# Performance work log

Measured on AMD Instinct MI355X. Metric: run time of the kernel, lower is better.

Reference implementation:

```python
import jax, jax.numpy as jnp
import numpy as np

N_NODES = 50000
N_EDGES = 800000
IN_CH = 64
HID = 128
OUT_CH = 1
NUM_LAYERS = 3
NUM_TIMESTEPS = 3
EDGE_DIM = 25
NUM_GRAPHS = 1024
NEG = 0.01  # leaky_relu negative slope (torch default & GATConv arg)


def leaky(v):
    return jnp.where(v >= 0, v, NEG * v)


def seg_softmax(a, idx, n):
    # PyG softmax: exp(a - max_per_segment) / (sum_per_segment + 1e-16)
    m = jax.ops.segment_max(a, idx, num_segments=n)
    m = jnp.where(jnp.isfinite(m), m, 0.0)  # guard empty segments
    e = jnp.exp(a - m[idx])
    s = jax.ops.segment_sum(e, idx, num_segments=n)
    return e / (s[idx] + 1e-16)


def gru(inp, h, Wih, Whh, bih, bhh):
    gi = inp @ Wih.T + bih
    gh = h @ Whh.T + bhh
    ir, iz, inn = jnp.split(gi, 3, axis=-1)
    hr, hz, hn = jnp.split(gh, 3, axis=-1)
    r = jax.nn.sigmoid(ir + hr)
    z = jax.nn.sigmoid(iz + hz)
    n = jnp.tanh(inn + r * hn)
    return (1.0 - z) * n + z * h


def setup_inputs() -> dict:
    key = jax.random.key(0)
    ks = iter(jax.random.split(key, 40))

    def nrm(shape, s=0.05):
        return jax.random.normal(next(ks), shape, dtype=jnp.float32) * s

    L = NUM_LAYERS - 1
    H3 = 3 * HID
    inp = dict(
        x=jax.random.normal(next(ks), (N_NODES, IN_CH), dtype=jnp.float32),
        edge_index=jax.random.randint(next(ks), (2, N_EDGES), 0, N_NODES),
        batch=jnp.sort(jax.random.randint(next(ks), (N_NODES,), 0, NUM_GRAPHS)),
        W1=nrm((HID, IN_CH)), b1=jnp.zeros((HID,), jnp.float32),
        Wg1=nrm((HID, HID + EDGE_DIM)), att_l=nrm((HID,)), att_r=nrm((HID,)),
        Wg2=nrm((HID, HID)), bg=jnp.zeros((HID,), jnp.float32),
        Wih0=nrm((H3, HID)), Whh0=nrm((H3, HID)),
        bih0=jnp.zeros((H3,), jnp.float32), bhh0=jnp.zeros((H3,), jnp.float32),
        Wa=nrm((L, HID, HID)), att_src_a=nrm((L, HID)), att_dst_a=nrm((L, HID)),
        ba=jnp.zeros((L, HID), jnp.float32),
        Wih_a=nrm((L, H3, HID)), Whh_a=nrm((L, H3, HID)),
        bih_a=jnp.zeros((L, H3), jnp.float32), bhh_a=jnp.zeros((L, H3), jnp.float32),
        Wm=nrm((HID, HID)), att_src_m=nrm((HID,)), att_dst_m=nrm((HID,)),
        bm=jnp.zeros((HID,), jnp.float32),
        Wih_m=nrm((H3, HID)), Whh_m=nrm((H3, HID)),
        bih_m=jnp.zeros((H3,), jnp.float32), bhh_m=jnp.zeros((H3,), jnp.float32),
        W2=nrm((OUT_CH, HID)), b2=jnp.zeros((OUT_CH,), jnp.float32),
    )
    return inp


def reference(x, edge_index, batch, W1, b1, Wg1, att_l, att_r, Wg2, bg,
              Wih0, Whh0, bih0, bhh0, Wa, att_src_a, att_dst_a, ba,
              Wih_a, Whh_a, bih_a, bhh_a, Wm, att_src_m, att_dst_m, bm,
              Wih_m, Whh_m, bih_m, bhh_m, W2, b2):
    N = x.shape[0]
    E = edge_index.shape[1]
    src, dst = edge_index[0], edge_index[1]  # j -> i, aggregate at i=dst
    edge_attr = jnp.ones((E, EDGE_DIM), dtype=x.dtype)  # built inside original forward

    x = leaky(x @ W1.T + b1)

    # GATEConv: edge-feature-aware attention, sum aggregation
    xe = leaky(jnp.concatenate([x[src], edge_attr], axis=-1) @ Wg1.T)  # [E, H]
    a = seg_softmax(leaky(xe @ att_l + (x @ att_r)[dst]), dst, N)
    msg = (x[src] @ Wg2.T) * a[:, None]
    h = jax.nn.elu(jax.ops.segment_sum(msg, dst, num_segments=N) + bg)
    x = jax.nn.relu(gru(h, x, Wih0, Whh0, bih0, bhh0))

    # (num_layers - 1) GATConv + GRU atom updates
    for l in range(NUM_LAYERS - 1):
        xt = x @ Wa[l].T
        a = seg_softmax(leaky((xt @ att_src_a[l])[src] + (xt @ att_dst_a[l])[dst]), dst, N)
        h = jax.nn.elu(jax.ops.segment_sum(xt[src] * a[:, None], dst, num_segments=N) + ba[l])
        x = jax.nn.relu(gru(h, x, Wih_a[l], Whh_a[l], bih_a[l], bhh_a[l]))

    # attentive readout: bipartite GATConv node->molecule over num_timesteps
    out = jax.nn.relu(jax.ops.segment_sum(x, batch, num_segments=NUM_GRAPHS))
    xt = x @ Wm.T                 # shared lin for src (fixed across timesteps)
    a_src = xt @ att_src_m        # [N]
    for _ in range(NUM_TIMESTEPS):
        ot = out @ Wm.T           # shared lin for dst
        a = seg_softmax(leaky(a_src + (ot @ att_dst_m)[batch]), batch, NUM_GRAPHS)
        h = jax.nn.elu(jax.ops.segment_sum(xt * a[:, None], batch, num_segments=NUM_GRAPHS) + bm)
        out = jax.nn.relu(gru(h, out, Wih_m, Whh_m, bih_m, bhh_m))

    return out @ W2.T + b2
```

## Files before the change

kernel.cpp:

```cpp
#include <hip/hip_runtime.h>
#include <math.h>

#define NN 50000
#define NE 800000
#define NG 1024
#define HID 128

typedef __attribute__((ext_vector_type(8))) short short8;
typedef __attribute__((ext_vector_type(4))) unsigned short ushort4v;
typedef __attribute__((ext_vector_type(4))) float f32x4;

__device__ __forceinline__ float leakyf(float v){ return v >= 0.f ? v : 0.01f*v; }
__device__ __forceinline__ float frcp(float x){ return __builtin_amdgcn_rcpf(x); }
__device__ __forceinline__ float fsigm(float v){ return frcp(1.f + __expf(-v)); }
__device__ __forceinline__ float ftanh(float v){ return 1.f - 2.f*frcp(1.f + __expf(2.f*v)); }
__device__ __forceinline__ float eluf(float v){ return v > 0.f ? v : __expf(v) - 1.f; }
__device__ __forceinline__ unsigned short bf16rne(float f){
  union { float f; unsigned u; } v; v.f = f;
  return (unsigned short)((v.u + 0x7FFFu + ((v.u >> 16) & 1u)) >> 16);
}
__device__ __forceinline__ float bf2f(unsigned short h){
  union { unsigned u; float f; } v; v.u = ((unsigned)h) << 16; return v.f;
}
__device__ __forceinline__ short8 cvt8(const float* a){
  short8 r;
#pragma unroll
  for (int j=0;j<8;j++) r[j] = (short)bf16rne(a[j]);
  return r;
}

__global__ __launch_bounds__(256)
void pack_all(const float* W1, const float* Wg1, const float* Wg2, const float* Wa,
              const float* Wm, const float* Wih0, const float* Whh0,
              const float* Wih_a, const float* Whh_a, const float* Wih_m,
              const float* Whh_m, unsigned short* __restrict__ dst)
{
  int m = (int)blockIdx.y;
  int t = (int)blockIdx.x*4 + ((int)threadIdx.x>>6);
  int l = (int)threadIdx.x & 63;
  const float* src; int stride=128, M=128, K=128; size_t doff;
  switch(m){
    case 0:  src=W1;    stride=64;  K=64;  doff=0;      break;
    case 1:  src=Wg1;   stride=153;        doff=8192;   break;
    case 2:  src=Wg2;                      doff=24576;  break;
    case 3:  src=Wa;                       doff=40960;  break;
    case 4:  src=Wa+16384;                 doff=57344;  break;
    case 5:  src=Wm;                       doff=73728;  break;
    case 6:  src=Wih0;  M=384;             doff=90112;  break;
    case 7:  src=Whh0;  M=384;             doff=139264; break;
    case 8:  src=Wih_a; M=384;             doff=188416; break;
    case 9:  src=Whh_a; M=384;             doff=237568; break;
    case 10: src=Wih_a+49152; M=384;       doff=286720; break;
    case 11: src=Whh_a+49152; M=384;       doff=335872; break;
    case 12: src=Wih_m; M=384;             doff=385024; break;
    default: src=Whh_m; M=384;             doff=434176; break;
  }
  int tk = K/32;
  if (t >= (M/16)*tk) return;
  int ct = t / tk, kc = t % tk;
  int row = ct*16 + (l&15);
  int col = kc*32 + ((l>>4)<<3);
  unsigned short o[8];
#pragma unroll
  for (int j=0;j<8;j++) o[j] = bf16rne(src[(size_t)row*stride + col + j]);
  ushort4v* d = (ushort4v*)(dst + doff + (((size_t)t*64 + l)<<3));
  ushort4v d0; d0.x=o[0]; d0.y=o[1]; d0.z=o[2]; d0.w=o[3];
  ushort4v d1; d1.x=o[4]; d1.y=o[5]; d1.z=o[6]; d1.w=o[7];
  d[0]=d0; d[1]=d1;
}

__global__ __launch_bounds__(256)
void gemm_f32(const float* __restrict__ A, const unsigned short* __restrict__ Wp,
              const float* __restrict__ bias, float* __restrict__ Cf,
              unsigned short* __restrict__ Cb, int rows, int act)
{
  constexpr int K = 64, KC = 2;
  const int tid=(int)threadIdx.x, w=tid>>6, l=tid&63;
  const int fr=l&15, fq=l>>4;
  const int rt=w>>1, ch=w&1;
  const int bn = (int)blockIdx.x*32;
  const int ar = bn + rt*16 + fr;
  f32x4 acc[4];
#pragma unroll
  for (int j=0;j<4;j++) acc[j] = (f32x4){0.f,0.f,0.f,0.f};
#pragma unroll
  for (int kc=0;kc<KC;kc++){
    float a8[8];
    if (ar < rows){
      *(float4*)&a8[0] = *(const float4*)(A + (size_t)ar*K + kc*32 + fq*8);
      *(float4*)&a8[4] = *(const float4*)(A + (size_t)ar*K + kc*32 + fq*8 + 4);
    } else {
#pragma unroll
      for (int j=0;j<8;j++) a8[j]=0.f;
    }
    short8 fa = cvt8(a8);
#pragma unroll
    for (int j=0;j<4;j++){
      const short8 bfr = *(const short8*)(Wp + ((((size_t)(ch*4+j)*KC + kc)*64 + l)<<3));
      acc[j] = __builtin_amdgcn_mfma_f32_16x16x32_bf16(fa, bfr, acc[j], 0, 0, 0);
    }
  }
#pragma unroll
  for (int j=0;j<4;j++){
    int c = ch*64 + j*16 + fr;
    float bv = bias ? bias[c] : 0.f;
#pragma unroll
    for (int r4=0;r4<4;r4++){
      float o = acc[j][r4] + bv;
      if (act) o = leakyf(o);
      int r = bn + rt*16 + fq*4 + r4;
      if (r < rows){
        Cf[(size_t)r*HID + c] = o;
        Cb[(size_t)r*HID + c] = bf16rne(o);
      }
    }
  }
}

__global__ __launch_bounds__(256)
void gemm_b16(const unsigned short* __restrict__ Ab, const unsigned short* __restrict__ Wp,
              const float* __restrict__ bias, unsigned short* __restrict__ Cb,
              const float* __restrict__ v1, const float* __restrict__ v2,
              float* __restrict__ s1, float* __restrict__ s2, int rows, int act)
{
  __shared__ float sd1[2][32];
  __shared__ float sd2[2][32];
  constexpr int KC = 4;
  const int tid=(int)threadIdx.x, w=tid>>6, l=tid&63;
  const int fr=l&15, fq=l>>4;
  const int rt=w>>1, ch=w&1;
  const int bn = (int)blockIdx.x*32;
  const int ar = bn + rt*16 + fr;
  f32x4 acc[4];
#pragma unroll
  for (int j=0;j<4;j++) acc[j] = (f32x4){0.f,0.f,0.f,0.f};
#pragma unroll
  for (int kc=0;kc<KC;kc++){
    short8 fa;
    if (ar < rows) fa = *(const short8*)(Ab + (size_t)ar*HID + kc*32 + fq*8);
    else { short8 z = {0,0,0,0,0,0,0,0}; fa = z; }
#pragma unroll
    for (int j=0;j<4;j++){
      const short8 bfr = *(const short8*)(Wp + ((((size_t)(ch*4+j)*KC + kc)*64 + l)<<3));
      acc[j] = __builtin_amdgcn_mfma_f32_16x16x32_bf16(fa, bfr, acc[j], 0, 0, 0);
    }
  }
  float dp1[4]={0.f,0.f,0.f,0.f}, dp2[4]={0.f,0.f,0.f,0.f};
#pragma unroll
  for (int j=0;j<4;j++){
    int c = ch*64 + j*16 + fr;
    float bv = bias ? bias[c] : 0.f;
    float w1 = v1 ? v1[c] : 0.f;
    float w2 = v2 ? v2[c] : 0.f;
#pragma unroll
    for (int r4=0;r4<4;r4++){
      float o = acc[j][r4] + bv;
      if (act) o = leakyf(o);
      dp1[r4] += o*w1; dp2[r4] += o*w2;
      int r = bn + rt*16 + fq*4 + r4;
      if (r < rows && Cb) Cb[(size_t)r*HID + c] = bf16rne(o);
    }
  }
  if (v1){
#pragma unroll
    for (int r4=0;r4<4;r4++){
#pragma unroll
      for (int m=1;m<16;m<<=1){ dp1[r4] += __shfl_xor(dp1[r4], m); dp2[r4] += __shfl_xor(dp2[r4], m); }
    }
    if (fr==0){
#pragma unroll
      for (int r4=0;r4<4;r4++){
        sd1[ch][rt*16 + fq*4 + r4] = dp1[r4];
        sd2[ch][rt*16 + fq*4 + r4] = dp2[r4];
      }
    }
    __syncthreads();
    if (tid < 32){
      int r = bn + tid;
      if (r < rows) s1[r] = sd1[0][tid] + sd1[1][tid];
    } else if (v2 && tid < 64){
      int r = bn + tid - 32;
      if (r < rows) s2[r] = sd2[0][tid-32] + sd2[1][tid-32];
    }
  }
}

__global__ __launch_bounds__(256)
void gemm_gate(const unsigned short* __restrict__ Ab,
               const unsigned short* __restrict__ W1p, const unsigned short* __restrict__ W2p,
               const float* __restrict__ cg, const float* __restrict__ attl,
               const float* __restrict__ attr,
               unsigned short* __restrict__ Cb,
               float* __restrict__ s1, float* __restrict__ s2, int rows)
{
  __shared__ float sd1[2][32];
  constexpr int KC = 4;
  const int tid=(int)threadIdx.x, w=tid>>6, l=tid&63;
  const int fr=l&15, fq=l>>4;
  const int rt=w>>1, ch=w&1;
  const int bn = (int)blockIdx.x*32;
  const int ar = bn + rt*16 + fr;
  f32x4 acc1[4], acc2[4];
#pragma unroll
  for (int j=0;j<4;j++){ acc1[j]=(f32x4){0,0,0,0}; acc2[j]=(f32x4){0,0,0,0}; }
  float pa = 0.f;
#pragma unroll
  for (int kc=0;kc<KC;kc++){
    short8 fa;
    if (ar < rows) fa = *(const short8*)(Ab + (size_t)ar*HID + kc*32 + fq*8);
    else { short8 z = {0,0,0,0,0,0,0,0}; fa = z; }
    if (ch==0){
      float4 t0 = *(const float4*)(attr + kc*32 + fq*8);
      float4 t1 = *(const float4*)(attr + kc*32 + fq*8 + 4);
      pa += bf2f((unsigned short)fa[0])*t0.x + bf2f((unsigned short)fa[1])*t0.y
          + bf2f((unsigned short)fa[2])*t0.z + bf2f((unsigned short)fa[3])*t0.w
          + bf2f((unsigned short)fa[4])*t1.x + bf2f((unsigned short)fa[5])*t1.y
          + bf2f((unsigned short)fa[6])*t1.z + bf2f((unsigned short)fa[7])*t1.w;
    }
#pragma unroll
    for (int j=0;j<4;j++){
      size_t wo = ((((size_t)(ch*4+j)*KC + kc)*64 + l)<<3);
      acc1[j] = __builtin_amdgcn_mfma_f32_16x16x32_bf16(fa, *(const short8*)(W1p + wo), acc1[j], 0, 0, 0);
      acc2[j] = __builtin_amdgcn_mfma_f32_16x16x32_bf16(fa, *(const short8*)(W2p + wo), acc2[j], 0, 0, 0);
    }
  }
  float dp1[4]={0.f,0.f,0.f,0.f};
#pragma unroll
  for (int j=0;j<4;j++){
    int c = ch*64 + j*16 + fr;
    float bv = cg[c];
    float w1 = attl[c];
#pragma unroll
    for (int r4=0;r4<4;r4++){
      float o1 = leakyf(acc1[j][r4] + bv);
      dp1[r4] += o1*w1;
      int r = bn + rt*16 + fq*4 + r4;
      if (r < rows) Cb[(size_t)r*HID + c] = bf16rne(acc2[j][r4]);
    }
  }
#pragma unroll
  for (int r4=0;r4<4;r4++){
#pragma unroll
    for (int m=1;m<16;m<<=1) dp1[r4] += __shfl_xor(dp1[r4], m);
  }
  if (fr==0){
#pragma unroll
    for (int r4=0;r4<4;r4++) sd1[ch][rt*16 + fq*4 + r4] = dp1[r4];
  }
  __syncthreads();
  if (tid < 32){
    int r = bn + tid;
    if (r < rows) s1[r] = sd1[0][tid] + sd1[1][tid];
  }
  if (ch==0){
    pa += __shfl_xor(pa, 16); pa += __shfl_xor(pa, 32);
    if (fq==0){
      int r = bn + rt*16 + fr;
      if (r < rows) s2[r] = pa;
    }
  }
}

#define GRU_TPB 4
__global__ __launch_bounds__(512, 2)
void fused_gru(const unsigned short* __restrict__ Ahb, const unsigned short* __restrict__ Axb,
               const float* __restrict__ Axf,
               const unsigned short* __restrict__ Wi, const unsigned short* __restrict__ Wh,
               const float* __restrict__ bih, const float* __restrict__ bhh,
               float* __restrict__ outf, unsigned short* __restrict__ outb, int tiles)
{
  const int tid=(int)threadIdx.x, w=tid>>6, l=tid&63;
  const int fr=l&15, fq=l>>4;
  short8 wi_r[3][4], wh_r[3][4];
#pragma unroll
  for (int g=0;g<3;g++)
#pragma unroll
    for (int kc=0;kc<4;kc++){
      size_t o = ((((size_t)(g*8 + w)*4 + kc)*64 + l)<<3);
      wi_r[g][kc] = *(const short8*)(Wi + o);
      wh_r[g][kc] = *(const short8*)(Wh + o);
    }
  const int c0 = w*16 + fr;
  float bi0=bih[c0], bi1=bih[c0+128], bi2=bih[c0+256];
  float bh0=bhh[c0], bh1=bhh[c0+128], bh2=bhh[c0+256];

  int rt = (int)blockIdx.x*GRU_TPB;
  int rt_end = min(rt + GRU_TPB, tiles);
  if (rt >= tiles) return;
  short8 fa[4], fx[4];
  {
    const int arow = rt*16 + fr;
#pragma unroll
    for (int kc=0;kc<4;kc++){
      fa[kc] = *(const short8*)(Ahb + (size_t)arow*HID + kc*32 + fq*8);
      fx[kc] = *(const short8*)(Axb + (size_t)arow*HID + kc*32 + fq*8);
    }
  }
  for (; rt < rt_end; rt++){
    short8 nfa[4], nfx[4];
    if (rt+1 < rt_end){
      const int arow = (rt+1)*16 + fr;
#pragma unroll
      for (int kc=0;kc<4;kc++){
        nfa[kc] = *(const short8*)(Ahb + (size_t)arow*HID + kc*32 + fq*8);
        nfx[kc] = *(const short8*)(Axb + (size_t)arow*HID + kc*32 + fq*8);
      }
    }
    float hv[4];
#pragma unroll
    for (int r4=0;r4<4;r4++) hv[r4] = Axf[(size_t)(rt*16 + fq*4 + r4)*HID + c0];

    f32x4 ai0={0,0,0,0}, ai1={0,0,0,0}, ai2={0,0,0,0};
    f32x4 ah0={0,0,0,0}, ah1={0,0,0,0}, ah2={0,0,0,0};
#pragma unroll
    for (int kc=0;kc<4;kc++){
      ai0 = __builtin_amdgcn_mfma_f32_16x16x32_bf16(fa[kc], wi_r[0][kc], ai0, 0, 0, 0);
      ai1 = __builtin_amdgcn_mfma_f32_16x16x32_bf16(fa[kc], wi_r[1][kc], ai1, 0, 0, 0);
      ai2 = __builtin_amdgcn_mfma_f32_16x16x32_bf16(fa[kc], wi_r[2][kc], ai2, 0, 0, 0);
      ah0 = __builtin_amdgcn_mfma_f32_16x16x32_bf16(fx[kc], wh_r[0][kc], ah0, 0, 0, 0);
      ah1 = __builtin_amdgcn_mfma_f32_16x16x32_bf16(fx[kc], wh_r[1][kc], ah1, 0, 0, 0);
      ah2 = __builtin_amdgcn_mfma_f32_16x16x32_bf16(fx[kc], wh_r[2][kc], ah2, 0, 0, 0);
    }
#pragma unroll
    for (int r4=0;r4<4;r4++){
      int row = rt*16 + fq*4 + r4;
      float rr = fsigm(ai0[r4] + bi0 + ah0[r4] + bh0);
      float zz = fsigm(ai1[r4] + bi1 + ah1[r4] + bh1);
      float nn = ftanh(ai2[r4] + bi2 + rr*(ah2[r4] + bh2));
      float o = fmaxf((1.f - zz)*nn + zz*hv[r4], 0.f);
      outf[(size_t)row*HID + c0] = o;
      outb[(size_t)row*HID + c0] = bf16rne(o);
    }
#pragma unroll
    for (int kc=0;kc<4;kc++){ fa[kc]=nfa[kc]; fx[kc]=nfx[kc]; }
  }
}

__global__ __launch_bounds__(256)
void rowdot(const float* __restrict__ A, const float* __restrict__ v,
            const float* __restrict__ bias, float* __restrict__ out, int rows)
{
  int wave = (int)((blockIdx.x * blockDim.x + threadIdx.x) >> 6);
  int lane = (int)(threadIdx.x & 63);
  if (wave >= rows) return;
  float2 a  = ((const float2*)(A + (size_t)wave*HID))[lane];
  float2 vv = ((const float2*)v)[lane];
  float s = a.x*vv.x + a.y*vv.y;
  for (int off=32; off; off>>=1) s += __shfl_down(s, off);
  if (lane==0) out[wave] = s + (bias ? bias[0] : 0.f);
}

__global__ void colvec(const float* __restrict__ W, const float* __restrict__ v,
                       float* __restrict__ out)
{
  int k = (int)threadIdx.x;
  float s = 0.f;
  for (int j=0;j<HID;j++) s += W[j*HID+k]*v[j];
  out[k] = s;
}

__global__ void prep_cg(const float* __restrict__ Wg1, float* __restrict__ cg){
  int j = (int)threadIdx.x;
  float s = 0.f;
  for (int k=128;k<153;k++) s += Wg1[j*153+k];
  cg[j] = s;
}

__global__ void count_kernel(const int* __restrict__ idx, int* __restrict__ cnt, int n){
  int i = (int)(blockIdx.x*blockDim.x + threadIdx.x);
  if (i < n) atomicAdd(&cnt[idx[i]], 1);
}

__global__ __launch_bounds__(1024)
void scan_blocks(const int* __restrict__ cnt, int* __restrict__ off,
                 int* __restrict__ tot, int n)
{
  __shared__ int buf[1024];
  int i = (int)(blockIdx.x*1024 + threadIdx.x);
  int v = (i<n)? cnt[i] : 0;
  buf[threadIdx.x] = v;
  __syncthreads();
  for (int s=1;s<1024;s<<=1){
    int t = ((int)threadIdx.x >= s) ? buf[threadIdx.x - s] : 0;
    __syncthreads();
    buf[threadIdx.x] += t;
    __syncthreads();
  }
  if (i<n) off[i] = buf[threadIdx.x] - v;
  if (threadIdx.x==1023) tot[blockIdx.x] = buf[1023];
}

__global__ void scan_tot(int* __restrict__ tot, int* __restrict__ off_end, int nb){
  int lane = (int)threadIdx.x;
  int orig = (lane<nb)? tot[lane] : 0;
  int v = orig;
  for (int s=1;s<64;s<<=1){ int t = __shfl_up(v, s); if (lane>=s) v += t; }
  int total = __shfl(v, 63);
  if (lane<nb) tot[lane] = v - orig;
  if (lane==0) *off_end = total;
}

__global__ void scan_add(int* __restrict__ off, const int* __restrict__ tot, int n){
  int i = (int)(blockIdx.x*blockDim.x + threadIdx.x);
  if (i<n) off[i] += tot[i>>10];
}

__global__ void fill_kernel(const int* __restrict__ src, const int* __restrict__ dst,
                            const int* __restrict__ off, int* __restrict__ fill,
                            int* __restrict__ ssrc, int n){
  int e = (int)(blockIdx.x*blockDim.x + threadIdx.x);
  if (e < n){
    int d = dst[e];
    int p = off[d] + atomicAdd(&fill[d], 1);
    __builtin_nontemporal_store(src[e], &ssrc[p]);
  }
}

__global__ void graph_bounds(const int* __restrict__ batch, int* __restrict__ goff){
  int g = (int)(blockIdx.x*blockDim.x + threadIdx.x);
  if (g > NG) return;
  int lo=0, hi=NN;
  while (lo<hi){ int mid=(lo+hi)>>1; if (batch[mid] < g) lo=mid+1; else hi=mid; }
  goff[g] = lo;
}

__global__ __launch_bounds__(256)
void agg_edges(const int* __restrict__ off, const int* __restrict__ ssrc,
               const float* __restrict__ ls, const float* __restrict__ ld,
               const unsigned short* __restrict__ Mrows, const float* __restrict__ bias,
               unsigned short* __restrict__ outb, int n)
{
  __shared__ float wbuf[4][64];
  __shared__ int   sbuf[4][64];
  const int ws = (int)(threadIdx.x >> 6);
  int node = (int)((blockIdx.x * blockDim.x + threadIdx.x) >> 6);
  int lane = (int)(threadIdx.x & 63);
  if (node >= n) return;
  int e0 = off[node], e1 = off[node+1];
  float ldv = ld[node];
  const int g4 = lane >> 4, cl = lane & 15;
  float denom = 0.f;
  float acc[8] = {0.f,0.f,0.f,0.f,0.f,0.f,0.f,0.f};
  for (int j0=e0; j0<e1; j0+=64){
    int cnt = min(64, e1-j0);
    float wv = 0.f; int sc = 0;
    if (lane < cnt){
      sc = ssrc[j0+lane];
      wv = __expf(leakyf(ls[sc]+ldv));
    }
    denom += wv;
    wbuf[ws][lane] = wv;
    sbuf[ws][lane] = sc;
#pragma unroll 2
    for (int k4=0;k4<cnt;k4+=4){
      float wk = wbuf[ws][k4+g4];
      int  sck = sbuf[ws][k4+g4];
      uint4 mm = *(const uint4*)(Mrows + (size_t)sck*HID + cl*8);
      acc[0] += wk*bf2f((unsigned short)(mm.x&0xffff));
      acc[1] += wk*bf2f((unsigned short)(mm.x>>16));
      acc[2] += wk*bf2f((unsigned short)(mm.y&0xffff));
      acc[3] += wk*bf2f((unsigned short)(mm.y>>16));
      acc[4] += wk*bf2f((unsigned short)(mm.z&0xffff));
      acc[5] += wk*bf2f((unsigned short)(mm.z>>16));
      acc[6] += wk*bf2f((unsigned short)(mm.w&0xffff));
      acc[7] += wk*bf2f((unsigned short)(mm.w>>16));
    }
  }
#pragma unroll
  for (int j=0;j<8;j++){ acc[j] += __shfl_xor(acc[j], 16); acc[j] += __shfl_xor(acc[j], 32); }
  for (int o=32;o;o>>=1) denom += __shfl_xor(denom, o);
  if (g4==0){
    float inv = frcp(denom + 1e-16f);
    float4 b0 = *(const float4*)(bias + cl*8);
    float4 b1 = *(const float4*)(bias + cl*8 + 4);
    float o0=eluf(acc[0]*inv+b0.x), o1=eluf(acc[1]*inv+b0.y);
    float o2=eluf(acc[2]*inv+b0.z), o3=eluf(acc[3]*inv+b0.w);
    float o4=eluf(acc[4]*inv+b1.x), o5=eluf(acc[5]*inv+b1.y);
    float o6=eluf(acc[6]*inv+b1.z), o7=eluf(acc[7]*inv+b1.w);
    uint4 u;
    u.x = (unsigned)bf16rne(o0) | ((unsigned)bf16rne(o1)<<16);
    u.y = (unsigned)bf16rne(o2) | ((unsigned)bf16rne(o3)<<16);
    u.z = (unsigned)bf16rne(o4) | ((unsigned)bf16rne(o5)<<16);
    u.w = (unsigned)bf16rne(o6) | ((unsigned)bf16rne(o7)<<16);
    *(uint4*)(outb + (size_t)node*HID + cl*8) = u;
  }
}

__global__ __launch_bounds__(128)
void graph_sum(const int* __restrict__ goff, const float* __restrict__ X,
               float* __restrict__ outf, unsigned short* __restrict__ outb)
{
  int g = (int)blockIdx.x;
  int c = (int)threadIdx.x;
  int n0 = goff[g], n1 = goff[g+1];
  float a0=0.f, a1=0.f, a2=0.f, a3=0.f;
  int n = n0;
  for (; n+4 <= n1; n += 4){
    a0 += X[(size_t)(n+0)*HID + c];
    a1 += X[(size_t)(n+1)*HID + c];
    a2 += X[(size_t)(n+2)*HID + c];
    a3 += X[(size_t)(n+3)*HID + c];
  }
  for (; n < n1; ++n) a0 += X[(size_t)n*HID + c];
  float o = fmaxf((a0+a1)+(a2+a3), 0.f);
  outf[(size_t)g*HID + c] = o;
  outb[(size_t)g*HID + c] = bf16rne(o);
}

__global__ __launch_bounds__(256)
void graph_soft2(const int* __restrict__ goff, const float* __restrict__ asrc,
                 const float* __restrict__ gout, const float* __restrict__ vmd,
                 const unsigned short* __restrict__ Xt, const float* __restrict__ bias,
                 unsigned short* __restrict__ outb)
{
  __shared__ float wbuf[4][64];
  const int ws = (int)(threadIdx.x >> 6);
  int g = (int)((blockIdx.x*blockDim.x + threadIdx.x) >> 6);
  int lane = (int)(threadIdx.x & 63);
  if (g >= NG) return;
  float2 ov = ((const float2*)(gout + (size_t)g*HID))[lane];
  float2 vv = ((const float2*)vmd)[lane];
  float ad = ov.x*vv.x + ov.y*vv.y;
  for (int o=32;o;o>>=1) ad += __shfl_xor(ad, o);
  int n0 = goff[g], n1 = goff[g+1];
  const int g4 = lane >> 4, cl = lane & 15;
  float denom = 0.f;
  float acc[8] = {0.f,0.f,0.f,0.f,0.f,0.f,0.f,0.f};
  for (int j0=n0; j0<n1; j0+=64){
    int cnt = min(64, n1-j0);
    float wv = 0.f;
    if (lane < cnt) wv = __expf(leakyf(asrc[j0+lane]+ad));
    denom += wv;
    wbuf[ws][lane] = wv;
#pragma unroll 2
    for (int k4=0;k4<cnt;k4+=4){
      float wk = wbuf[ws][k4+g4];
      int rowi = min(j0 + k4 + g4, n1 - 1);
      uint4 mm = *(const uint4*)(Xt + (size_t)rowi*HID + cl*8);
      acc[0] += wk*bf2f((unsigned short)(mm.x&0xffff));
      acc[1] += wk*bf2f((unsigned short)(mm.x>>16));
      acc[2] += wk*bf2f((unsigned short)(mm.y&0xffff));
      acc[3] += wk*bf2f((unsigned short)(mm.y>>16));
      acc[4] += wk*bf2f((unsigned short)(mm.z&0xffff));
      acc[5] += wk*bf2f((unsigned short)(mm.z>>16));
      acc[6] += wk*bf2f((unsigned short)(mm.w&0xffff));
      acc[7] += wk*bf2f((unsigned short)(mm.w>>16));
    }
  }
#pragma unroll
  for (int j=0;j<8;j++){ acc[j] += __shfl_xor(acc[j], 16); acc[j] += __shfl_xor(acc[j], 32); }
  for (int o=32;o;o>>=1) denom += __shfl_xor(denom, o);
  if (g4==0){
    float inv = frcp(denom + 1e-16f);
    float4 b0 = *(const float4*)(bias + cl*8);
    float4 b1 = *(const float4*)(bias + cl*8 + 4);
    float o0=eluf(acc[0]*inv+b0.x), o1=eluf(acc[1]*inv+b0.y);
    float o2=eluf(acc[2]*inv+b0.z), o3=eluf(acc[3]*inv+b0.w);
    float o4=eluf(acc[4]*inv+b1.x), o5=eluf(acc[5]*inv+b1.y);
    float o6=eluf(acc[6]*inv+b1.z), o7=eluf(acc[7]*inv+b1.w);
    uint4 u;
    u.x = (unsigned)bf16rne(o0) | ((unsigned)bf16rne(o1)<<16);
    u.y = (unsigned)bf16rne(o2) | ((unsigned)bf16rne(o3)<<16);
    u.z = (unsigned)bf16rne(o4) | ((unsigned)bf16rne(o5)<<16);
    u.w = (unsigned)bf16rne(o6) | ((unsigned)bf16rne(o7)<<16);
    *(uint4*)(outb + (size_t)g*HID + cl*8) = u;
  }
}

extern "C" void kernel_launch(void* const* d_in, const int* in_sizes, int n_in,
                              void* d_out, int out_size, void* d_ws, size_t ws_size,
                              hipStream_t stream)
{
  const float* x_in  = (const float*)d_in[0];
  const int*   ei    = (const int*)d_in[1];
  const int*   batch = (const int*)d_in[2];
  const float* W1    = (const float*)d_in[3];
  const float* b1    = (const float*)d_in[4];
  const float* Wg1   = (const float*)d_in[5];
  const float* att_l = (const float*)d_in[6];
  const float* att_r = (const float*)d_in[7];
  const float* Wg2   = (const float*)d_in[8];
  const float* bg    = (const float*)d_in[9];
  const float* Wih0  = (const float*)d_in[10];
  const float* Whh0  = (const float*)d_in[11];
  const float* bih0  = (const float*)d_in[12];
  const float* bhh0  = (const float*)d_in[13];
  const float* Wa    = (const float*)d_in[14];
  const float* att_src_a = (const float*)d_in[15];
  const float* att_dst_a = (const float*)d_in[16];
  const float* ba    = (const float*)d_in[17];
  const float* Wih_a = (const float*)d_in[18];
  const float* Whh_a = (const float*)d_in[19];
  const float* bih_a = (const float*)d_in[20];
  const float* bhh_a = (const float*)d_in[21];
  const float* Wm    = (const float*)d_in[22];
  const float* att_src_m = (const float*)d_in[23];
  const float* att_dst_m = (const float*)d_in[24];
  const float* bm    = (const float*)d_in[25];
  const float* Wih_m = (const float*)d_in[26];
  const float* Whh_m = (const float*)d_in[27];
  const float* bih_m = (const float*)d_in[28];
  const float* bhh_m = (const float*)d_in[29];
  const float* W2    = (const float*)d_in[30];
  const float* b2    = (const float*)d_in[31];
  (void)in_sizes; (void)n_in; (void)out_size; (void)ws_size;

  char* wsb = (char*)d_ws;
  size_t off = 0;
  auto alloc = [&](size_t bytes)->void* {
    void* p = wsb + off;
    off += (bytes + 255) & ~(size_t)255;
    return p;
  };
  float* f_x   = (float*)alloc((size_t)NN*HID*4);
  float* f_y   = (float*)alloc((size_t)NN*HID*4);
  unsigned short* f_xb = (unsigned short*)alloc((size_t)NN*HID*2);
  unsigned short* f_yb = (unsigned short*)alloc((size_t)NN*HID*2);
  unsigned short* f_h  = (unsigned short*)alloc((size_t)NN*HID*2);
  unsigned short* f_t  = (unsigned short*)alloc((size_t)NN*HID*2);
  float* f_s1  = (float*)alloc((size_t)NN*4);
  float* f_s2  = (float*)alloc((size_t)NN*4);
  float* g_of0 = (float*)alloc((size_t)NG*HID*4);
  float* g_of1 = (float*)alloc((size_t)NG*HID*4);
  unsigned short* g_ob0 = (unsigned short*)alloc((size_t)NG*HID*2);
  unsigned short* g_ob1 = (unsigned short*)alloc((size_t)NG*HID*2);
  unsigned short* g_hb  = (unsigned short*)alloc((size_t)NG*HID*2);
  float* w_cg  = (float*)alloc((size_t)HID*4);
  float* w_vmd = (float*)alloc((size_t)HID*4);
  unsigned short* w_pack = (unsigned short*)alloc((size_t)483328*2);
  int* i_cnt   = (int*)alloc((size_t)NN*4);
  int* i_off   = (int*)alloc((size_t)(NN+1)*4);
  int* i_fill  = (int*)alloc((size_t)NN*4);
  int* i_src   = (int*)alloc((size_t)NE*4);
  int* i_tot   = (int*)alloc((size_t)64*4);
  int* i_goff  = (int*)alloc((size_t)(NG+1)*4);

  const unsigned short* pk_W1   = w_pack + 0;
  const unsigned short* pk_g1   = w_pack + 8192;
  const unsigned short* pk_g2   = w_pack + 24576;
  const unsigned short* pk_wa0  = w_pack + 40960;
  const unsigned short* pk_wa1  = w_pack + 57344;
  const unsigned short* pk_wm   = w_pack + 73728;
  const unsigned short* pk_wih0 = w_pack + 90112;
  const unsigned short* pk_whh0 = w_pack + 139264;
  const unsigned short* pk_wiha0= w_pack + 188416;
  const unsigned short* pk_whha0= w_pack + 237568;
  const unsigned short* pk_wiha1= w_pack + 286720;
  const unsigned short* pk_whha1= w_pack + 335872;
  const unsigned short* pk_wihm = w_pack + 385024;
  const unsigned short* pk_whhm = w_pack + 434176;

  const int* e_src = ei;
  const int* e_dst = ei + NE;

  hipMemsetAsync(i_cnt, 0, (size_t)NN*4, stream);
  hipMemsetAsync(i_fill, 0, (size_t)NN*4, stream);

  const int NB = (NN + 1023)/1024;
  count_kernel<<<(NE+255)/256,256,0,stream>>>(e_dst, i_cnt, NE);
  scan_blocks<<<NB,1024,0,stream>>>(i_cnt, i_off, i_tot, NN);
  scan_tot<<<1,64,0,stream>>>(i_tot, i_off+NN, NB);
  scan_add<<<(NN+255)/256,256,0,stream>>>(i_off, i_tot, NN);
  fill_kernel<<<(NE+255)/256,256,0,stream>>>(e_src, e_dst, i_off, i_fill, i_src, NE);
  graph_bounds<<<(NG+1+255)/256,256,0,stream>>>(batch, i_goff);
  prep_cg<<<1,128,0,stream>>>(Wg1, w_cg);
  colvec<<<1,128,0,stream>>>(Wm, att_dst_m, w_vmd);
  pack_all<<<dim3(24,14),256,0,stream>>>(W1, Wg1, Wg2, Wa, Wm, Wih0, Whh0,
                                         Wih_a, Whh_a, Wih_m, Whh_m, w_pack);

  const int GB = (NN+31)/32;
  const int NT = NN/16;
  const int FB = (NT+GRU_TPB-1)/GRU_TPB;
  const int GT = NG/16;
  const int wavegrid_g = (NG*64)/256;

  gemm_f32<<<GB,256,0,stream>>>(x_in, pk_W1, b1, f_x, f_xb, NN, 1);

  float* curf = f_x;  unsigned short* curb = f_xb;
  float* nxtf = f_y;  unsigned short* nxtb = f_yb;

  gemm_gate<<<GB,256,0,stream>>>(curb, pk_g1, pk_g2, w_cg, att_l, att_r,
                                 f_t, f_s1, f_s2, NN);
  agg_edges<<<(NN+3)/4,256,0,stream>>>(i_off, i_src, f_s1, f_s2, f_t, bg, f_h, NN);
  fused_gru<<<FB,512,0,stream>>>(f_h, curb, curf, pk_wih0, pk_whh0, bih0, bhh0,
                                 nxtf, nxtb, NT);
  { float* t=curf; curf=nxtf; nxtf=t; unsigned short* tb=curb; curb=nxtb; nxtb=tb; }

  for (int l=0;l<2;l++){
    gemm_b16<<<GB,256,0,stream>>>(curb, l ? pk_wa1 : pk_wa0, nullptr, f_t,
                                  att_src_a + l*HID, att_dst_a + l*HID,
                                  f_s1, f_s2, NN, 0);
    agg_edges<<<(NN+3)/4,256,0,stream>>>(i_off, i_src, f_s1, f_s2, f_t, ba + l*HID, f_h, NN);
    fused_gru<<<FB,512,0,stream>>>(f_h, curb, curf,
                                   l ? pk_wiha1 : pk_wiha0, l ? pk_whha1 : pk_whha0,
                                   bih_a + l*384, bhh_a + l*384, nxtf, nxtb, NT);
    { float* t=curf; curf=nxtf; nxtf=t; unsigned short* tb=curb; curb=nxtb; nxtb=tb; }
  }

  graph_sum<<<NG,128,0,stream>>>(i_goff, curf, g_of0, g_ob0);
  gemm_b16<<<GB,256,0,stream>>>(curb, pk_wm, nullptr, f_t,
                                att_src_m, nullptr, f_s1, nullptr, NN, 0);
  float* gcf = g_of0; unsigned short* gcb = g_ob0;
  float* gnf = g_of1; unsigned short* gnb = g_ob1;
  for (int t=0;t<3;t++){
    graph_soft2<<<wavegrid_g,256,0,stream>>>(i_goff, f_s1, gcf, w_vmd, f_t, bm, g_hb);
    fused_gru<<<(GT+GRU_TPB-1)/GRU_TPB,512,0,stream>>>(g_hb, gcb, gcf, pk_wihm, pk_whhm,
                                                       bih_m, bhh_m, gnf, gnb, GT);
    { float* tf=gcf; gcf=gnf; gnf=tf; unsigned short* tb=gcb; gcb=gnb; gnb=tb; }
  }

  rowdot<<<wavegrid_g,256,0,stream>>>(gcf, W2, b2, (float*)d_out, NG);
}
```

Measured before the change: 620.4 us.

## Fuse attentive readout timesteps, GRU and output into one per-graph kernel

After: 618.6 us. No clear change (-0.3%).

```diff
diff --git a/kernel.cpp b/kernel.cpp
--- a/kernel.cpp
+++ b/kernel.cpp
@@ -32,8 +32,8 @@
 __global__ __launch_bounds__(256)
 void pack_all(const float* W1, const float* Wg1, const float* Wg2, const float* Wa,
               const float* Wm, const float* Wih0, const float* Whh0,
-              const float* Wih_a, const float* Whh_a, const float* Wih_m,
-              const float* Whh_m, unsigned short* __restrict__ dst)
+              const float* Wih_a, const float* Whh_a,
+              unsigned short* __restrict__ dst)
 {
   int m = (int)blockIdx.y;
   int t = (int)blockIdx.x*4 + ((int)threadIdx.x>>6);
@@ -51,9 +51,7 @@
     case 8:  src=Wih_a; M=384;             doff=188416; break;
     case 9:  src=Whh_a; M=384;             doff=237568; break;
     case 10: src=Wih_a+49152; M=384;       doff=286720; break;
-    case 11: src=Whh_a+49152; M=384;       doff=335872; break;
-    case 12: src=Wih_m; M=384;             doff=385024; break;
-    default: src=Whh_m; M=384;             doff=434176; break;
+    default: src=Whh_a+49152; M=384;       doff=335872; break;
   }
   int tk = K/32;
   if (t >= (M/16)*tk) return;
@@ -67,6 +65,15 @@
   ushort4v d0; d0.x=o[0]; d0.y=o[1]; d0.z=o[2]; d0.w=o[3];
   ushort4v d1; d1.x=o[4]; d1.y=o[5]; d1.z=o[6]; d1.w=o[7];
   d[0]=d0; d[1]=d1;
+}
+
+__global__ void pack_t(const float* __restrict__ Wi, const float* __restrict__ Wh,
+                       unsigned short* __restrict__ Wit, unsigned short* __restrict__ Wht)
+{
+  int k = (int)blockIdx.x;
+  int cg = (int)threadIdx.x + (int)blockIdx.y*128;
+  Wit[(size_t)k*384 + cg] = bf16rne(Wi[(size_t)cg*128 + k]);
+  Wht[(size_t)k*384 + cg] = bf16rne(Wh[(size_t)cg*128 + k]);
 }
 
 __global__ __launch_bounds__(256)
@@ -336,20 +343,6 @@
   }
 }
 
-__global__ __launch_bounds__(256)
-void rowdot(const float* __restrict__ A, const float* __restrict__ v,
-            const float* __restrict__ bias, float* __restrict__ out, int rows)
-{
-  int wave = (int)((blockIdx.x * blockDim.x + threadIdx.x) >> 6);
-  int lane = (int)(threadIdx.x & 63);
-  if (wave >= rows) return;
-  float2 a  = ((const float2*)(A + (size_t)wave*HID))[lane];
-  float2 vv = ((const float2*)v)[lane];
-  float s = a.x*vv.x + a.y*vv.y;
-  for (int off=32; off; off>>=1) s += __shfl_down(s, off);
-  if (lane==0) out[wave] = s + (bias ? bias[0] : 0.f);
-}
-
 __global__ void colvec(const float* __restrict__ W, const float* __restrict__ v,
                        float* __restrict__ out)
 {
@@ -400,19 +393,22 @@
   if (lane==0) *off_end = total;
 }
 
-__global__ void scan_add(int* __restrict__ off, const int* __restrict__ tot, int n){
+__global__ void scan_add(int* __restrict__ off, int* __restrict__ off_mut,
+                         const int* __restrict__ tot, int n){
   int i = (int)(blockIdx.x*blockDim.x + threadIdx.x);
-  if (i<n) off[i] += tot[i>>10];
+  if (i<n){
+    int v = off[i] + tot[i>>10];
+    off[i] = v;
+    off_mut[i] = v;
+  }
 }
 
 __global__ void fill_kernel(const int* __restrict__ src, const int* __restrict__ dst,
-                            const int* __restrict__ off, int* __restrict__ fill,
-                            int* __restrict__ ssrc, int n){
+                            int* __restrict__ off_mut, int* __restrict__ ssrc, int n){
   int e = (int)(blockIdx.x*blockDim.x + threadIdx.x);
   if (e < n){
-    int d = dst[e];
-    int p = off[d] + atomicAdd(&fill[d], 1);
-    __builtin_nontemporal_store(src[e], &ssrc[p]);
+    int p = atomicAdd(&off_mut[dst[e]], 1);
+    ssrc[p] = src[e];
   }
 }
 
@@ -487,84 +483,65 @@
 }
 
 __global__ __launch_bounds__(128)
-void graph_sum(const int* __restrict__ goff, const float* __restrict__ X,
-               float* __restrict__ outf, unsigned short* __restrict__ outb)
-{
-  int g = (int)blockIdx.x;
-  int c = (int)threadIdx.x;
-  int n0 = goff[g], n1 = goff[g+1];
-  float a0=0.f, a1=0.f, a2=0.f, a3=0.f;
+void readout_all(const int* __restrict__ goff, const float* __restrict__ X,
+                 const float* __restrict__ asrc, const unsigned short* __restrict__ Xt,
+                 const float* __restrict__ vmd, const float* __restrict__ bm_,
+                 const unsigned short* __restrict__ Wit, const unsigned short* __restrict__ Wht,
+                 const float* __restrict__ bih, const float* __restrict__ bhh,
+                 const float* __restrict__ W2, const float* __restrict__ b2,
+                 float* __restrict__ dout)
+{
+  __shared__ float sh_h[128];
+  __shared__ float sh_o[128];
+  __shared__ float sred[2];
+  const int g = (int)blockIdx.x, c = (int)threadIdx.x;
+  const int n0 = goff[g], n1 = goff[g+1];
+  float a0=0.f,a1=0.f,a2=0.f,a3=0.f;
   int n = n0;
-  for (; n+4 <= n1; n += 4){
-    a0 += X[(size_t)(n+0)*HID + c];
-    a1 += X[(size_t)(n+1)*HID + c];
-    a2 += X[(size_t)(n+2)*HID + c];
-    a3 += X[(size_t)(n+3)*HID + c];
-  }
-  for (; n < n1; ++n) a0 += X[(size_t)n*HID + c];
-  float o = fmaxf((a0+a1)+(a2+a3), 0.f);
-  outf[(size_t)g*HID + c] = o;
-  outb[(size_t)g*HID + c] = bf16rne(o);
-}
-
-__global__ __launch_bounds__(256)
-void graph_soft2(const int* __restrict__ goff, const float* __restrict__ asrc,
-                 const float* __restrict__ gout, const float* __restrict__ vmd,
-                 const unsigned short* __restrict__ Xt, const float* __restrict__ bias,
-                 unsigned short* __restrict__ outb)
-{
-  __shared__ float wbuf[4][64];
-  const int ws = (int)(threadIdx.x >> 6);
-  int g = (int)((blockIdx.x*blockDim.x + threadIdx.x) >> 6);
-  int lane = (int)(threadIdx.x & 63);
-  if (g >= NG) return;
-  float2 ov = ((const float2*)(gout + (size_t)g*HID))[lane];
-  float2 vv = ((const float2*)vmd)[lane];
-  float ad = ov.x*vv.x + ov.y*vv.y;
-  for (int o=32;o;o>>=1) ad += __shfl_xor(ad, o);
-  int n0 = goff[g], n1 = goff[g+1];
-  const int g4 = lane >> 4, cl = lane & 15;
-  float denom = 0.f;
-  float acc[8] = {0.f,0.f,0.f,0.f,0.f,0.f,0.f,0.f};
-  for (int j0=n0; j0<n1; j0+=64){
-    int cnt = min(64, n1-j0);
-    float wv = 0.f;
-    if (lane < cnt) wv = __expf(leakyf(asrc[j0+lane]+ad));
-    denom += wv;
-    wbuf[ws][lane] = wv;
-#pragma unroll 2
-    for (int k4=0;k4<cnt;k4+=4){
-      float wk = wbuf[ws][k4+g4];
-      int rowi = min(j0 + k4 + g4, n1 - 1);
-      uint4 mm = *(const uint4*)(Xt + (size_t)rowi*HID + cl*8);
-      acc[0] += wk*bf2f((unsigned short)(mm.x&0xffff));
-      acc[1] += wk*bf2f((unsigned short)(mm.x>>16));
-      acc[2] += wk*bf2f((unsigned short)(mm.y&0xffff));
-      acc[3] += wk*bf2f((unsigned short)(mm.y>>16));
-      acc[4] += wk*bf2f((unsigned short)(mm.z&0xffff));
-      acc[5] += wk*bf2f((unsigned short)(mm.z>>16));
-      acc[6] += wk*bf2f((unsigned short)(mm.w&0xffff));
-      acc[7] += wk*bf2f((unsigned short)(mm.w>>16));
-    }
-  }
-#pragma unroll
-  for (int j=0;j<8;j++){ acc[j] += __shfl_xor(acc[j], 16); acc[j] += __shfl_xor(acc[j], 32); }
-  for (int o=32;o;o>>=1) denom += __shfl_xor(denom, o);
-  if (g4==0){
-    float inv = frcp(denom + 1e-16f);
-    float4 b0 = *(const float4*)(bias + cl*8);
-    float4 b1 = *(const float4*)(bias + cl*8 + 4);
-    float o0=eluf(acc[0]*inv+b0.x), o1=eluf(acc[1]*inv+b0.y);
-    float o2=eluf(acc[2]*inv+b0.z), o3=eluf(acc[3]*inv+b0.w);
-    float o4=eluf(acc[4]*inv+b1.x), o5=eluf(acc[5]*inv+b1.y);
-    float o6=eluf(acc[6]*inv+b1.z), o7=eluf(acc[7]*inv+b1.w);
-    uint4 u;
-    u.x = (unsigned)bf16rne(o0) | ((unsigned)bf16rne(o1)<<16);
-    u.y = (unsigned)bf16rne(o2) | ((unsigned)bf16rne(o3)<<16);
-    u.z = (unsigned)bf16rne(o4) | ((unsigned)bf16rne(o5)<<16);
-    u.w = (unsigned)bf16rne(o6) | ((unsigned)bf16rne(o7)<<16);
-    *(uint4*)(outb + (size_t)g*HID + cl*8) = u;
-  }
+  for (; n+4<=n1; n+=4){
+    a0 += X[(size_t)(n+0)*HID+c]; a1 += X[(size_t)(n+1)*HID+c];
+    a2 += X[(size_t)(n+2)*HID+c]; a3 += X[(size_t)(n+3)*HID+c];
+  }
+  for (; n<n1; ++n) a0 += X[(size_t)n*HID+c];
+  float ov = fmaxf((a0+a1)+(a2+a3), 0.f);
+  const float bi0=bih[c], bi1=bih[c+128], bi2=bih[c+256];
+  const float bh0=bhh[c], bh1=bhh[c+128], bh2=bhh[c+256];
+  const float vm = vmd[c], bmc = bm_[c];
+  for (int t=0;t<3;t++){
+    float p = ov*vm;
+    for (int o=32;o;o>>=1) p += __shfl_down(p, o);
+    if ((c&63)==0) sred[c>>6] = p;
+    __syncthreads();
+    float ad = sred[0] + sred[1];
+    float denom = 0.f, acc = 0.f;
+    for (int nn=n0; nn<n1; ++nn){
+      float wv = __expf(leakyf(asrc[nn] + ad));
+      denom += wv;
+      acc += wv * bf2f(Xt[(size_t)nn*HID + c]);
+    }
+    float h = eluf(acc*frcp(denom + 1e-16f) + bmc);
+    __syncthreads();
+    sh_h[c] = h; sh_o[c] = ov;
+    __syncthreads();
+    float gi0=0.f,gi1=0.f,gi2=0.f,gh0=0.f,gh1=0.f,gh2=0.f;
+    for (int k=0;k<128;k++){
+      float hk = sh_h[k], ok = sh_o[k];
+      const unsigned short* wi = Wit + (size_t)k*384;
+      const unsigned short* wh = Wht + (size_t)k*384;
+      gi0 += bf2f(wi[c])*hk;  gi1 += bf2f(wi[c+128])*hk;  gi2 += bf2f(wi[c+256])*hk;
+      gh0 += bf2f(wh[c])*ok;  gh1 += bf2f(wh[c+128])*ok;  gh2 += bf2f(wh[c+256])*ok;
+    }
+    float rr = fsigm(gi0+bi0+gh0+bh0);
+    float zz = fsigm(gi1+bi1+gh1+bh1);
+    float nv = ftanh(gi2+bi2 + rr*(gh2+bh2));
+    ov = fmaxf((1.f-zz)*nv + zz*ov, 0.f);
+  }
+  float p = ov*W2[c];
+  for (int o=32;o;o>>=1) p += __shfl_down(p, o);
+  __syncthreads();
+  if ((c&63)==0) sred[c>>6] = p;
+  __syncthreads();
+  if (c==0) dout[g] = sred[0] + sred[1] + b2[0];
 }
 
 extern "C" void kernel_launch(void* const* d_in, const int* in_sizes, int n_in,
@@ -620,17 +597,14 @@
   unsigned short* f_t  = (unsigned short*)alloc((size_t)NN*HID*2);
   float* f_s1  = (float*)alloc((size_t)NN*4);
   float* f_s2  = (float*)alloc((size_t)NN*4);
-  float* g_of0 = (float*)alloc((size_t)NG*HID*4);
-  float* g_of1 = (float*)alloc((size_t)NG*HID*4);
-  unsigned short* g_ob0 = (unsigned short*)alloc((size_t)NG*HID*2);
-  unsigned short* g_ob1 = (unsigned short*)alloc((size_t)NG*HID*2);
-  unsigned short* g_hb  = (unsigned short*)alloc((size_t)NG*HID*2);
   float* w_cg  = (float*)alloc((size_t)HID*4);
   float* w_vmd = (float*)alloc((size_t)HID*4);
-  unsigned short* w_pack = (unsigned short*)alloc((size_t)483328*2);
+  unsigned short* w_pack = (unsigned short*)alloc((size_t)385024*2);
+  unsigned short* w_wit  = (unsigned short*)alloc((size_t)49152*2);
+  unsigned short* w_wht  = (unsigned short*)alloc((size_t)49152*2);
   int* i_cnt   = (int*)alloc((size_t)NN*4);
   int* i_off   = (int*)alloc((size_t)(NN+1)*4);
-  int* i_fill  = (int*)alloc((size_t)NN*4);
+  int* i_offm  = (int*)alloc((size_t)NN*4);
   int* i_src   = (int*)alloc((size_t)NE*4);
   int* i_tot   = (int*)alloc((size_t)64*4);
   int* i_goff  = (int*)alloc((size_t)(NG+1)*4);
@@ -647,32 +621,28 @@
   const unsigned short* pk_whha0= w_pack + 237568;
   const unsigned short* pk_wiha1= w_pack + 286720;
   const unsigned short* pk_whha1= w_pack + 335872;
-  const unsigned short* pk_wihm = w_pack + 385024;
-  const unsigned short* pk_whhm = w_pack + 434176;
 
   const int* e_src = ei;
   const int* e_dst = ei + NE;
 
   hipMemsetAsync(i_cnt, 0, (size_t)NN*4, stream);
-  hipMemsetAsync(i_fill, 0, (size_t)NN*4, stream);
 
   const int NB = (NN + 1023)/1024;
   count_kernel<<<(NE+255)/256,256,0,stream>>>(e_dst, i_cnt, NE);
   scan_blocks<<<NB,1024,0,stream>>>(i_cnt, i_off, i_tot, NN);
   scan_tot<<<1,64,0,stream>>>(i_tot, i_off+NN, NB);
-  scan_add<<<(NN+255)/256,256,0,stream>>>(i_off, i_tot, NN);
-  fill_kernel<<<(NE+255)/256,256,0,stream>>>(e_src, e_dst, i_off, i_fill, i_src, NE);
+  scan_add<<<(NN+255)/256,256,0,stream>>>(i_off, i_offm, i_tot, NN);
+  fill_kernel<<<(NE+255)/256,256,0,stream>>>(e_src, e_dst, i_offm, i_src, NE);
   graph_bounds<<<(NG+1+255)/256,256,0,stream>>>(batch, i_goff);
   prep_cg<<<1,128,0,stream>>>(Wg1, w_cg);
   colvec<<<1,128,0,stream>>>(Wm, att_dst_m, w_vmd);
-  pack_all<<<dim3(24,14),256,0,stream>>>(W1, Wg1, Wg2, Wa, Wm, Wih0, Whh0,
-                                         Wih_a, Whh_a, Wih_m, Whh_m, w_pack);
+  pack_all<<<dim3(24,12),256,0,stream>>>(W1, Wg1, Wg2, Wa, Wm, Wih0, Whh0,
+                                         Wih_a, Whh_a, w_pack);
+  pack_t<<<dim3(128,3),128,0,stream>>>(Wih_m, Whh_m, w_wit, w_wht);
 
   const int GB = (NN+31)/32;
   const int NT = NN/16;
   const int FB = (NT+GRU_TPB-1)/GRU_TPB;
-  const int GT = NG/16;
-  const int wavegrid_g = (NG*64)/256;
 
   gemm_f32<<<GB,256,0,stream>>>(x_in, pk_W1, b1, f_x, f_xb, NN, 1);
 
@@ -697,17 +667,9 @@
     { float* t=curf; curf=nxtf; nxtf=t; unsigned short* tb=curb; curb=nxtb; nxtb=tb; }
   }
 
-  graph_sum<<<NG,128,0,stream>>>(i_goff, curf, g_of0, g_ob0);
   gemm_b16<<<GB,256,0,stream>>>(curb, pk_wm, nullptr, f_t,
                                 att_src_m, nullptr, f_s1, nullptr, NN, 0);
-  float* gcf = g_of0; unsigned short* gcb = g_ob0;
-  float* gnf = g_of1; unsigned short* gnb = g_ob1;
-  for (int t=0;t<3;t++){
-    graph_soft2<<<wavegrid_g,256,0,stream>>>(i_goff, f_s1, gcf, w_vmd, f_t, bm, g_hb);
-    fused_gru<<<(GT+GRU_TPB-1)/GRU_TPB,512,0,stream>>>(g_hb, gcb, gcf, pk_wihm, pk_whhm,
-                                                       bih_m, bhh_m, gnf, gnb, GT);
-    { float* tf=gcf; gcf=gnf; gnf=tf; unsigned short* tb=gcb; gcb=gnb; gnb=tb; }
-  }
-
-  rowdot<<<wavegrid_g,256,0,stream>>>(gcf, W2, b2, (float*)d_out, NG);
-}
+  readout_all<<<NG,128,0,stream>>>(i_goff, curf, f_s1, f_t, w_vmd, bm,
+                                   w_wit, w_wht, bih_m, bhh_m, W2, b2,
+                                   (float*)d_out);
+}
```
